# Kernel tuning notes

Measured on AMD Instinct MI355X. Metric: run time of the kernel, lower is better.

Reference implementation:

```python
import jax, jax.numpy as jnp
import numpy as np
from math import factorial

# (mul, l, parity) for in1 == in2 == out
IRREPS = [(32, 0, 1), (32, 1, -1), (32, 2, 1)]
FEAT_DIM = sum(m * (2 * l + 1) for m, l, _ in IRREPS)  # 288
BATCH = 8192


def _cg(j1, m1, j2, m2, j3, m3):
    # Clebsch-Gordan <j1 m1 j2 m2 | j3 m3> (Racah formula), complex SH basis
    if m1 + m2 != m3 or not (abs(j1 - j2) <= j3 <= j1 + j2):
        return 0.0
    f = factorial
    pre = (2 * j3 + 1) * f(j3 + j1 - j2) * f(j3 - j1 + j2) * f(j1 + j2 - j3) / f(j1 + j2 + j3 + 1)
    pre *= f(j3 + m3) * f(j3 - m3) * f(j1 - m1) * f(j1 + m1) * f(j2 - m2) * f(j2 + m2)
    s = 0.0
    for k in range(0, j1 + j2 - j3 + 1):
        a = [k, j1 + j2 - j3 - k, j1 - m1 - k, j2 + m2 - k, j3 - j2 + m1 + k, j3 - j1 - m2 + k]
        if min(a) < 0:
            continue
        s += (-1.0) ** k / (f(a[0]) * f(a[1]) * f(a[2]) * f(a[3]) * f(a[4]) * f(a[5]))
    return np.sqrt(pre) * s


def _q(l):
    # unitary change of basis: real SH coords = Q @ complex SH coords
    Q = np.zeros((2 * l + 1, 2 * l + 1), dtype=np.complex128)
    Q[l, l] = 1.0
    for m in range(1, l + 1):
        Q[l + m, l + m] = (-1.0) ** m / np.sqrt(2.0)
        Q[l + m, l - m] = 1.0 / np.sqrt(2.0)
        Q[l - m, l - m] = 1j / np.sqrt(2.0)
        Q[l - m, l + m] = -1j * (-1.0) ** m / np.sqrt(2.0)
    return Q


def _wigner3j(l1, l2, l3):
    # real-basis Wigner 3j tensor, unit Frobenius norm (e3nn convention up to sign)
    C = np.zeros((2 * l1 + 1, 2 * l2 + 1, 2 * l3 + 1), dtype=np.complex128)
    for m1 in range(-l1, l1 + 1):
        for m2 in range(-l2, l2 + 1):
            m3 = -(m1 + m2)
            if abs(m3) <= l3:
                C[m1 + l1, m2 + l2, m3 + l3] = (-1.0) ** (l1 - l2 - m3) * _cg(l1, m1, l2, m2, l3, -m3)
    T = np.einsum('mnp,am,bn,cp->abc', C, _q(l1).conj(), _q(l2).conj(), _q(l3).conj())
    T = T.real if np.abs(T.real).sum() >= np.abs(T.imag).sum() else T.imag
    return (T / np.linalg.norm(T)).astype(np.float32)


def _instructions():
    # all parity- and triangle-allowed fully-connected 'uvw' paths
    ins = []
    for i1, (m1, l1, p1) in enumerate(IRREPS):
        for i2, (m2, l2, p2) in enumerate(IRREPS):
            for io, (mo, lo, po) in enumerate(IRREPS):
                if p1 * p2 == po and abs(l1 - l2) <= lo <= l1 + l2:
                    ins.append((i1, i2, io))
    return ins


N_WEIGHT = sum(IRREPS[i1][0] * IRREPS[i2][0] * IRREPS[io][0] for i1, i2, io in _instructions())  # 360448


def setup_inputs() -> dict:
    key = jax.random.key(0)
    k1, k2, k3 = jax.random.split(key, 3)
    return {
        'x1': jax.random.normal(k1, (BATCH, FEAT_DIM), jnp.float32),
        'x2': jax.random.normal(k2, (BATCH, FEAT_DIM), jnp.float32),
        'weight': jax.random.normal(k3, (N_WEIGHT,), jnp.float32),
    }


def _tp(x1, x2, weight):
    ins = _instructions()
    fan = {}
    for i1, i2, io in ins:  # 'element' path normalization fan-in per output irrep
        fan[io] = fan.get(io, 0) + IRREPS[i1][0] * IRREPS[i2][0]
    offs, o = [], 0
    for m, l, _ in IRREPS:
        offs.append(o)
        o += m * (2 * l + 1)
    z = x1.shape[0]
    out = [jnp.zeros((z, m * (2 * l + 1)), x1.dtype) for m, l, _ in IRREPS]
    w_off = 0
    for i1, i2, io in ins:
        m1, l1, _ = IRREPS[i1]
        m2, l2, _ = IRREPS[i2]
        mo, lo, _ = IRREPS[io]
        x1p = x1[:, offs[i1]:offs[i1] + m1 * (2 * l1 + 1)].reshape(z, m1, 2 * l1 + 1)
        x2p = x2[:, offs[i2]:offs[i2] + m2 * (2 * l2 + 1)].reshape(z, m2, 2 * l2 + 1)
        nw = m1 * m2 * mo
        W = weight[w_off:w_off + nw].reshape(m1, m2, mo)
        w_off += nw
        w3 = jnp.asarray(_wigner3j(l1, l2, lo))
        alpha = float(np.sqrt((2 * lo + 1) / fan[io]))  # component norm * 1/sqrt(fan_in)
        # contraction order chosen to keep intermediates small:
        t = jnp.einsum('zui,uvw->zivw', x1p, W)             # [z, 2l1+1, m2, mo]
        y = jnp.einsum('zivw,zvj,ijk->zwk', t, x2p, w3, optimize='optimal')
        out[io] = out[io] + alpha * y.reshape(z, -1)
    return jnp.concatenate(out, axis=1)


def reference(x1, x2, weight):
    return _tp(x1, x2, weight)
```

## Files before the change

### kernel.cpp

```cpp
#include <hip/hip_runtime.h>


__device__ float g_w3[11 * 128];


__device__ __forceinline__ double dfact(int n) {
    double r = 1.0;
    for (int i = 2; i <= n; ++i) r *= (double)i;
    return r;
}

__device__ double cg_coef(int j1, int m1, int j2, int m2, int j3, int m3) {
    if (m1 + m2 != m3) return 0.0;
    int lo = (j1 > j2) ? (j1 - j2) : (j2 - j1);
    if (j3 > j1 + j2 || j3 < lo) return 0.0;
    double pre = (2.0 * j3 + 1.0) * dfact(j3 + j1 - j2) * dfact(j3 - j1 + j2) *
                 dfact(j1 + j2 - j3) / dfact(j1 + j2 + j3 + 1);
    pre *= dfact(j3 + m3) * dfact(j3 - m3) * dfact(j1 - m1) * dfact(j1 + m1) *
           dfact(j2 - m2) * dfact(j2 + m2);
    double s = 0.0;
    for (int k = 0; k <= j1 + j2 - j3; ++k) {
        int a1 = j1 + j2 - j3 - k, a2 = j1 - m1 - k, a3 = j2 + m2 - k;
        int a4 = j3 - j2 + m1 + k, a5 = j3 - j1 - m2 + k;
        if (a1 < 0 || a2 < 0 || a3 < 0 || a4 < 0 || a5 < 0) continue;
        double t = 1.0 / (dfact(k) * dfact(a1) * dfact(a2) * dfact(a3) * dfact(a4) * dfact(a5));
        s += (k & 1) ? -t : t;
    }
    return sqrt(pre) * s;
}

__device__ __forceinline__ void qval(int l, int a, int mi, double& re, double& im) {
    re = 0.0; im = 0.0;
    const double inv = 0.7071067811865475244;
    int ma = a - l, mc = mi - l;
    if (ma == 0) { if (mc == 0) re = 1.0; return; }
    if (ma > 0) {
        if (mc == ma)        re = (ma & 1) ? -inv : inv;
        else if (mc == -ma)  re = inv;
    } else {
        int mm = -ma;
        if (mc == ma)        im = inv;
        else if (mc == -ma)  im = -((mm & 1) ? -inv : inv);
    }
}

__global__ void wigner3j_setup() {
    const int L1[11] = {0,0,0,1,1,1,1,2,2,2,2};
    const int L2[11] = {0,1,2,0,1,1,2,0,1,2,2};
    const int L3[11] = {0,1,2,1,0,2,1,2,1,0,2};
    const int p = blockIdx.x;
    const int l1 = L1[p], l2 = L2[p], l3 = L3[p];
    const int d1 = 2 * l1 + 1, d2 = 2 * l2 + 1, d3 = 2 * l3 + 1;
    const int n = d1 * d2 * d3;

    __shared__ double sre[125], sim[125];
    __shared__ double s_scale;
    __shared__ int s_im;

    const int e = threadIdx.x;
    if (e < n) {
        int a = e / (d2 * d3);
        int r = e - a * d2 * d3;
        int b = r / d3;
        int c = r - b * d3;
        double tre = 0.0, tim = 0.0;
        for (int m1 = -l1; m1 <= l1; ++m1) {
            for (int m2 = -l2; m2 <= l2; ++m2) {
                int m3 = -(m1 + m2);
                if (m3 < -l3 || m3 > l3) continue;
                int ex = l1 - l2 - m3;
                double sgn = (ex % 2 != 0) ? -1.0 : 1.0;
                double C = sgn * cg_coef(l1, m1, l2, m2, l3, -m3);
                if (C == 0.0) continue;
                double r1, i1, r2, i2, r3, i3;
                qval(l1, a, m1 + l1, r1, i1);
                qval(l2, b, m2 + l2, r2, i2);
                qval(l3, c, m3 + l3, r3, i3);
                i1 = -i1; i2 = -i2; i3 = -i3;
                double rr = r1 * r2 - i1 * i2;
                double ri = r1 * i2 + i1 * r2;
                double fr = rr * r3 - ri * i3;
                double fi = rr * i3 + ri * r3;
                tre += C * fr;
                tim += C * fi;
            }
        }
        sre[e] = tre; sim[e] = tim;
    }
    __syncthreads();
    if (threadIdx.x == 0) {
        double sar = 0.0, sai = 0.0;
        for (int i = 0; i < n; ++i) { sar += fabs(sre[i]); sai += fabs(sim[i]); }
        int useim = (sar >= sai) ? 0 : 1;
        double ss = 0.0;
        for (int i = 0; i < n; ++i) { double v = useim ? sim[i] : sre[i]; ss += v * v; }
        s_scale = 1.0 / sqrt(ss);
        s_im = useim;
    }
    __syncthreads();
    if (e < n) {
        double v = s_im ? sim[e] : sre[e];
        g_w3[p * 128 + e] = (float)(v * s_scale);
    }
}


template <int DH, int DS, int D1, int D2, int DO, bool HX1, int NW>
__device__ __forceinline__ void do_path(const float* __restrict__ xh,
                                        const float* __restrict__ xs,
                                        const float* __restrict__ Wp,
                                        const float* __restrict__ w3p,
                                        int k, float* __restrict__ acc) {
    float w3l[DH][DS];
#pragma unroll
    for (int ih = 0; ih < DH; ++ih) {
#pragma unroll
        for (int is = 0; is < DS; ++is) {
            const int i = HX1 ? ih : is;
            const int j = HX1 ? is : ih;
            w3l[ih][is] = w3p[(i * D2 + j) * DO + k];
        }
    }
    constexpr int CH = (DH >= 5) ? 16 : 32;
#pragma unroll 1
    for (int h0 = 0; h0 < 32; h0 += CH) {
        float H[CH * DH];
#pragma unroll
        for (int h = 0; h < CH; ++h) {
#pragma unroll
            for (int i = 0; i < DH; ++i) H[h * DH + i] = xh[(h0 + h) * DH + i];
        }
#pragma unroll 1
        for (int s = 0; s < 32; ++s) {
            float b[DS];
#pragma unroll
            for (int j = 0; j < DS; ++j) b[j] = xs[s * DS + j];
            float c[DH];
#pragma unroll
            for (int i = 0; i < DH; ++i) {
                float t = 0.f;
#pragma unroll
                for (int j = 0; j < DS; ++j) t = fmaf(w3l[i][j], b[j], t);
                c[i] = t;
            }
            const float* wbase = Wp + (HX1 ? s * 32 : s * 1024);
#pragma unroll
            for (int h = 0; h < CH; ++h) {
                float o = 0.f;
#pragma unroll
                for (int i = 0; i < DH; ++i) o = fmaf(c[i], H[h * DH + i], o);
                const float* wr = wbase + (HX1 ? (h0 + h) * 1024 : (h0 + h) * 32);
#pragma unroll
                for (int w = 0; w < NW; ++w) acc[w] = fmaf(wr[w], o, acc[w]);
            }
        }
    }
}

__global__ __launch_bounds__(64, 2) void tp_main(const float* __restrict__ x1,
                                                 const float* __restrict__ x2,
                                                 const float* __restrict__ W,
                                                 float* __restrict__ out) {
    const int z = blockIdx.x * 64 + threadIdx.x;
    const float* r1 = x1 + (size_t)z * 288;
    const float* r2 = x2 + (size_t)z * 288;
    const int w0 = blockIdx.z * 16;
    const float* w3t = g_w3;

    float acc[16];
#pragma unroll
    for (int i = 0; i < 16; ++i) acc[i] = 0.f;

    const int arm = blockIdx.y;
    int io, k;
    if (arm == 0)      { io = 0; k = 0; }
    else if (arm <= 3) { io = 1; k = arm - 1; }
    else               { io = 2; k = arm - 4; }

    if (io == 0) {
        do_path<1, 1, 1, 1, 1, false, 16>(r2 + 0,   r1 + 0,   W + 0 * 32768 + w0,  w3t + 0 * 128, 0, acc);
        do_path<3, 3, 3, 3, 1, false, 16>(r2 + 32,  r1 + 32,  W + 4 * 32768 + w0,  w3t + 4 * 128, 0, acc);
        do_path<5, 5, 5, 5, 1, false, 16>(r2 + 128, r1 + 128, W + 9 * 32768 + w0,  w3t + 9 * 128, 0, acc);
    } else if (io == 1) {
        do_path<1, 3, 1, 3, 3, true,  16>(r1 + 0,   r2 + 32,  W + 1 * 32768 + w0,  w3t + 1 * 128, k, acc);
        do_path<1, 3, 3, 1, 3, false, 16>(r2 + 0,   r1 + 32,  W + 3 * 32768 + w0,  w3t + 3 * 128, k, acc);
        do_path<3, 5, 3, 5, 3, true,  16>(r1 + 32,  r2 + 128, W + 6 * 32768 + w0,  w3t + 6 * 128, k, acc);
        do_path<3, 5, 5, 3, 3, false, 16>(r2 + 32,  r1 + 128, W + 8 * 32768 + w0,  w3t + 8 * 128, k, acc);
    } else {
        do_path<1, 5, 1, 5, 5, true,  16>(r1 + 0,   r2 + 128, W + 2 * 32768 + w0,  w3t + 2 * 128, k, acc);
        do_path<3, 3, 3, 3, 5, false, 16>(r2 + 32,  r1 + 32,  W + 5 * 32768 + w0,  w3t + 5 * 128, k, acc);
        do_path<1, 5, 5, 1, 5, false, 16>(r2 + 0,   r1 + 128, W + 7 * 32768 + w0,  w3t + 7 * 128, k, acc);
        do_path<5, 5, 5, 5, 5, false, 16>(r2 + 128, r1 + 128, W + 10 * 32768 + w0, w3t + 10 * 128, k, acc);
    }

    const float alpha = (io == 0) ? 0.018042196f : ((io == 1) ? 0.027063294f : 0.034938562f);
    const int off_o   = (io == 0) ? 0 : ((io == 1) ? 32 : 128);
    const int DOd     = (io == 0) ? 1 : ((io == 1) ? 3 : 5);
    float* orow = out + (size_t)z * 288 + off_o + k;
#pragma unroll
    for (int w = 0; w < 16; ++w) orow[(w0 + w) * DOd] = alpha * acc[w];
}


extern "C" void kernel_launch(void* const* d_in, const int* in_sizes, int n_in,
                              void* d_out, int out_size, void* d_ws, size_t ws_size,
                              hipStream_t stream) {
    const float* x1 = (const float*)d_in[0];
    const float* x2 = (const float*)d_in[1];
    const float* W  = (const float*)d_in[2];
    float* out = (float*)d_out;

    wigner3j_setup<<<dim3(11), dim3(128), 0, stream>>>();
    tp_main<<<dim3(128, 9, 2), dim3(64), 0, stream>>>(x1, x2, W, out);
}
```

Measured before the change: 400.7 us.

## Transpose inputs to feature-major layout for coalesced per-thread feature loads

Adds a shared-memory tiled transpose kernel that writes x1 and x2 into workspace in feature-major order with a padded row stride. The main kernel is templated on stride, so adjacent threads (adjacent batch rows) read consecutive addresses instead of rows 288 floats apart. This targets uncoalesced global loads of the input features in the inner loops, at the cost of an extra launch and a full read and write of both inputs. It falls back to the original layout when the workspace is too small.

Result: slower. 956.2 us (+138.6%).

```diff
diff --git a/kernel.cpp b/kernel.cpp
--- a/kernel.cpp
+++ b/kernel.cpp
@@ -2,6 +2,8 @@
 
 
 __device__ float g_w3[11 * 128];
+
+constexpr int PZ = 8192 + 64;
 
 
 __device__ __forceinline__ double dfact(int n) {
@@ -105,7 +107,27 @@
 }
 
 
-template <int DH, int DS, int D1, int D2, int DO, bool HX1, int NW>
+__global__ void transpose_x(const float* __restrict__ x1,
+                            const float* __restrict__ x2,
+                            float* __restrict__ ws) {
+    __shared__ float tile[32][33];
+    const float* in = (blockIdx.z == 0) ? x1 : x2;
+    float* outT = ws + (size_t)blockIdx.z * 288 * PZ;
+    const int f0 = blockIdx.x * 32;
+    const int z0 = blockIdx.y * 32;
+    const int tx = threadIdx.x;
+    const int ty = threadIdx.y;
+#pragma unroll
+    for (int i = 0; i < 32; i += 8)
+        tile[ty + i][tx] = in[(size_t)(z0 + ty + i) * 288 + f0 + tx];
+    __syncthreads();
+#pragma unroll
+    for (int i = 0; i < 32; i += 8)
+        outT[(size_t)(f0 + ty + i) * PZ + z0 + tx] = tile[tx][ty + i];
+}
+
+
+template <int DH, int DS, int D1, int D2, int DO, bool HX1, int NW, int STRIDE>
 __device__ __forceinline__ void do_path(const float* __restrict__ xh,
                                         const float* __restrict__ xs,
                                         const float* __restrict__ Wp,
@@ -128,13 +150,14 @@
 #pragma unroll
         for (int h = 0; h < CH; ++h) {
 #pragma unroll
-            for (int i = 0; i < DH; ++i) H[h * DH + i] = xh[(h0 + h) * DH + i];
+            for (int i = 0; i < DH; ++i)
+                H[h * DH + i] = xh[(size_t)((h0 + h) * DH + i) * STRIDE];
         }
 #pragma unroll 1
         for (int s = 0; s < 32; ++s) {
             float b[DS];
 #pragma unroll
-            for (int j = 0; j < DS; ++j) b[j] = xs[s * DS + j];
+            for (int j = 0; j < DS; ++j) b[j] = xs[(size_t)(s * DS + j) * STRIDE];
             float c[DH];
 #pragma unroll
             for (int i = 0; i < DH; ++i) {
@@ -157,13 +180,21 @@
     }
 }
 
+template <int STRIDE>
 __global__ __launch_bounds__(64, 2) void tp_main(const float* __restrict__ x1,
                                                  const float* __restrict__ x2,
                                                  const float* __restrict__ W,
                                                  float* __restrict__ out) {
     const int z = blockIdx.x * 64 + threadIdx.x;
-    const float* r1 = x1 + (size_t)z * 288;
-    const float* r2 = x2 + (size_t)z * 288;
+    const float* r1;
+    const float* r2;
+    if (STRIDE == 1) {
+        r1 = x1 + (size_t)z * 288;
+        r2 = x2 + (size_t)z * 288;
+    } else {
+        r1 = x1 + z;
+        r2 = x2 + z;
+    }
     const int w0 = blockIdx.z * 16;
     const float* w3t = g_w3;
 
@@ -178,19 +209,19 @@
     else               { io = 2; k = arm - 4; }
 
     if (io == 0) {
-        do_path<1, 1, 1, 1, 1, false, 16>(r2 + 0,   r1 + 0,   W + 0 * 32768 + w0,  w3t + 0 * 128, 0, acc);
-        do_path<3, 3, 3, 3, 1, false, 16>(r2 + 32,  r1 + 32,  W + 4 * 32768 + w0,  w3t + 4 * 128, 0, acc);
-        do_path<5, 5, 5, 5, 1, false, 16>(r2 + 128, r1 + 128, W + 9 * 32768 + w0,  w3t + 9 * 128, 0, acc);
+        do_path<1, 1, 1, 1, 1, false, 16, STRIDE>(r2,                r1,                W + 0 * 32768 + w0,  w3t + 0 * 128, 0, acc);
+        do_path<3, 3, 3, 3, 1, false, 16, STRIDE>(r2 + 32 * STRIDE,  r1 + 32 * STRIDE,  W + 4 * 32768 + w0,  w3t + 4 * 128, 0, acc);
+        do_path<5, 5, 5, 5, 1, false, 16, STRIDE>(r2 + 128 * STRIDE, r1 + 128 * STRIDE, W + 9 * 32768 + w0,  w3t + 9 * 128, 0, acc);
     } else if (io == 1) {
-        do_path<1, 3, 1, 3, 3, true,  16>(r1 + 0,   r2 + 32,  W + 1 * 32768 + w0,  w3t + 1 * 128, k, acc);
-        do_path<1, 3, 3, 1, 3, false, 16>(r2 + 0,   r1 + 32,  W + 3 * 32768 + w0,  w3t + 3 * 128, k, acc);
-        do_path<3, 5, 3, 5, 3, true,  16>(r1 + 32,  r2 + 128, W + 6 * 32768 + w0,  w3t + 6 * 128, k, acc);
-        do_path<3, 5, 5, 3, 3, false, 16>(r2 + 32,  r1 + 128, W + 8 * 32768 + w0,  w3t + 8 * 128, k, acc);
-    } else {
-        do_path<1, 5, 1, 5, 5, true,  16>(r1 + 0,   r2 + 128, W + 2 * 32768 + w0,  w3t + 2 * 128, k, acc);
-        do_path<3, 3, 3, 3, 5, false, 16>(r2 + 32,  r1 + 32,  W + 5 * 32768 + w0,  w3t + 5 * 128, k, acc);
-        do_path<1, 5, 5, 1, 5, false, 16>(r2 + 0,   r1 + 128, W + 7 * 32768 + w0,  w3t + 7 * 128, k, acc);
-        do_path<5, 5, 5, 5, 5, false, 16>(r2 + 128, r1 + 128, W + 10 * 32768 + w0, w3t + 10 * 128, k, acc);
+        do_path<1, 3, 1, 3, 3, true,  16, STRIDE>(r1,                r2 + 32 * STRIDE,  W + 1 * 32768 + w0,  w3t + 1 * 128, k, acc);
+        do_path<1, 3, 3, 1, 3, false, 16, STRIDE>(r2,                r1 + 32 * STRIDE,  W + 3 * 32768 + w0,  w3t + 3 * 128, k, acc);
+        do_path<3, 5, 3, 5, 3, true,  16, STRIDE>(r1 + 32 * STRIDE,  r2 + 128 * STRIDE, W + 6 * 32768 + w0,  w3t + 6 * 128, k, acc);
+        do_path<3, 5, 5, 3, 3, false, 16, STRIDE>(r2 + 32 * STRIDE,  r1 + 128 * STRIDE, W + 8 * 32768 + w0,  w3t + 8 * 128, k, acc);
+    } else {
+        do_path<1, 5, 1, 5, 5, true,  16, STRIDE>(r1,                r2 + 128 * STRIDE, W + 2 * 32768 + w0,  w3t + 2 * 128, k, acc);
+        do_path<3, 3, 3, 3, 5, false, 16, STRIDE>(r2 + 32 * STRIDE,  r1 + 32 * STRIDE,  W + 5 * 32768 + w0,  w3t + 5 * 128, k, acc);
+        do_path<1, 5, 5, 1, 5, false, 16, STRIDE>(r2,                r1 + 128 * STRIDE, W + 7 * 32768 + w0,  w3t + 7 * 128, k, acc);
+        do_path<5, 5, 5, 5, 5, false, 16, STRIDE>(r2 + 128 * STRIDE, r1 + 128 * STRIDE, W + 10 * 32768 + w0, w3t + 10 * 128, k, acc);
     }
 
     const float alpha = (io == 0) ? 0.018042196f : ((io == 1) ? 0.027063294f : 0.034938562f);
@@ -211,5 +242,14 @@
     float* out = (float*)d_out;
 
     wigner3j_setup<<<dim3(11), dim3(128), 0, stream>>>();
-    tp_main<<<dim3(128, 9, 2), dim3(64), 0, stream>>>(x1, x2, W, out);
-}
+
+    const size_t need = (size_t)2 * 288 * PZ * sizeof(float);
+    if (ws_size >= need) {
+        float* x1T = (float*)d_ws;
+        float* x2T = x1T + (size_t)288 * PZ;
+        transpose_x<<<dim3(9, 256, 2), dim3(32, 8), 0, stream>>>(x1, x2, (float*)d_ws);
+        tp_main<PZ><<<dim3(128, 9, 2), dim3(64), 0, stream>>>(x1T, x2T, W, out);
+    } else {
+        tp_main<1><<<dim3(128, 9, 2), dim3(64), 0, stream>>>(x1, x2, W, out);
+    }
+}
```
